# Performance work log

Measured on AMD Instinct MI355X. Metric: run time of the kernel, lower is better.

Reference implementation:

```python
import jax, jax.numpy as jnp
import numpy as np

GAM1 = 1.0
GAM2 = 1.0
EPS = 0.01


def setup_inputs() -> dict:
    key = jax.random.key(0)
    k1, k2 = jax.random.split(key)
    m, p, k = 262144, 128, 10
    x = jax.random.normal(k1, (m, p), dtype=jnp.float32)
    y = jax.random.randint(k2, (m,), 0, k, dtype=jnp.int32)
    return {"x": x, "y": y, "num_classes": k}


def reference(x, y, num_classes):
    m, p = x.shape
    I = jnp.eye(p, dtype=x.dtype)
    scalar = p / (m * EPS)

    # W = x.T, so W @ W.T == x.T @ x  (p x p Gram)
    cov = x.T @ x
    discrimn_empi = jnp.linalg.slogdet(I + GAM1 * scalar * cov)[1] / 2.0
    discrimn_theo = jnp.linalg.slogdet(I + scalar * cov)[1] / 2.0

    # per-class compress loss: logdet(I + p/(n_j*eps) * W_j W_j^T) * n_j / m
    onehot = jax.nn.one_hot(y, num_classes, dtype=x.dtype)  # [m, k]
    counts = onehot.sum(axis=0)                             # [k]

    def class_cov(col):  # col: [m] 0/1 mask for one class
        return (x * col[:, None]).T @ x  # [p, p]

    covs = jax.lax.map(class_cov, onehot.T)  # [k, p, p], sequential over k classes

    safe_counts = jnp.maximum(counts, 1.0)
    scal = p / (safe_counts * EPS)                              # [k]
    lds = jnp.linalg.slogdet(I[None] + scal[:, None, None] * covs)[1]  # [k]
    compress = jnp.sum(jnp.where(counts > 0, lds * counts / m, 0.0)) / 2.0

    total_loss_empi = GAM2 * (-discrimn_empi) + compress
    return total_loss_empi, discrimn_empi, discrimn_theo, compress
```

## Files before the change

kernel.cpp:

```cpp
#include <hip/hip_runtime.h>

#define K 10
#define P 128
#define EPSV 0.01f
#define GAM1 1.0f
#define GAM2 1.0f
#define CH 512
#define SK 64
#define KS 68
#define NSTG (CH / SK)
#define SORTCH 2048
#define NTHR 256
#define GTHR 512

typedef __attribute__((ext_vector_type(8))) short bf16x8;
typedef __attribute__((ext_vector_type(4))) short s16x4;
typedef __attribute__((ext_vector_type(4))) float f32x4;

static __device__ __forceinline__ short f2bf(float f) {
    unsigned u = __float_as_uint(f);
    u = (u + 0x7FFFu + ((u >> 16) & 1u)) >> 16;
    return (short)u;
}

static __device__ __forceinline__ float rdlane(float v, int srclane) {
    return __int_as_float(__builtin_amdgcn_readlane(__float_as_int(v), srclane));
}

__global__ void hist_kernel(const int* __restrict__ y, int* __restrict__ blk_counts, int m) {
    __shared__ int h[K];
    int t = threadIdx.x;
    if (t < K) h[t] = 0;
    __syncthreads();
    int base = blockIdx.x * SORTCH;
    int rows = min(SORTCH, m - base);
    for (int i = t; i < rows; i += NTHR) atomicAdd(&h[y[base + i]], 1);
    __syncthreads();
    if (t < K) blk_counts[blockIdx.x * K + t] = h[t];
}

__global__ void scan_kernel(const int* __restrict__ blk_counts, int* __restrict__ blk_offsets,
                            int* __restrict__ counts, int* __restrict__ pstart, int nb) {
    __shared__ int s[K][128];
    __shared__ int sps[K + 1];
    int t = threadIdx.x;
    int own[K];
    if (t < 128) {
        for (int c = 0; c < K; ++c) {
            int v = (t < nb) ? blk_counts[t * K + c] : 0;
            own[c] = v;
            s[c][t] = v;
        }
    }
    __syncthreads();
    for (int off = 1; off < 128; off <<= 1) {
        int tmp[K];
        if (t < 128)
            for (int c = 0; c < K; ++c) tmp[c] = (t >= off) ? s[c][t - off] : 0;
        __syncthreads();
        if (t < 128)
            for (int c = 0; c < K; ++c) s[c][t] += tmp[c];
        __syncthreads();
    }
    if (t == 0) {
        int run = 0;
        for (int c = 0; c < K; ++c) {
            sps[c] = run;
            int tot = s[c][127];
            counts[c] = tot;
            pstart[c] = run;
            run += ((tot + CH - 1) / CH) * CH;
        }
        sps[K] = run;
        pstart[K] = run;
    }
    __syncthreads();
    if (t < nb)
        for (int c = 0; c < K; ++c)
            blk_offsets[t * K + c] = sps[c] + s[c][t] - own[c];
}

__global__ void scatter_kernel(const int* __restrict__ y, const int* __restrict__ blk_offsets,
                               int* __restrict__ perm, int m) {
    __shared__ int cur[K];
    int t = threadIdx.x;
    if (t < K) cur[t] = blk_offsets[blockIdx.x * K + t];
    __syncthreads();
    int base = blockIdx.x * SORTCH;
    int rows = min(SORTCH, m - base);
    for (int i = t; i < rows; i += NTHR) {
        int row = base + i;
        int pos = atomicAdd(&cur[y[row]], 1);
        perm[pos] = row;
    }
}

__global__ __launch_bounds__(GTHR, 4) void gram_kernel(const float* __restrict__ x,
                                                       const int* __restrict__ perm,
                                                       const int* __restrict__ pstart,
                                                       const int* __restrict__ counts,
                                                       float* __restrict__ partial) {
    __shared__ int pm[CH];
    __shared__ short xsT[2][P * KS];
    int t = threadIdx.x;
    int base = blockIdx.x * CH;
    int cls = 0;
#pragma unroll
    for (int c = 1; c < K; ++c)
        if (base >= pstart[c]) cls = c;
    const int limit = pstart[cls] + counts[cls];
    pm[t] = perm[base + t];

    const int lane = t & 63;
    const int wave = t >> 6;
    const int m16 = lane & 15;
    const int quad = lane >> 4;
    const int wr = wave >> 1;
    const int wc = wave & 1;
    const int c2 = lane;

    f32x4 acc[2][4];
#pragma unroll
    for (int a = 0; a < 2; ++a)
#pragma unroll
        for (int b = 0; b < 4; ++b) acc[a][b] = (f32x4){0.f, 0.f, 0.f, 0.f};

    __syncthreads();

    float2 v[8];
#pragma unroll
    for (int ii = 0; ii < 8; ++ii) {
        int pos = wave * 8 + ii;
        float2 val; val.x = 0.f; val.y = 0.f;
        if (base + pos < limit) {
            int r = pm[pos];
            val = ((const float2*)(x + (size_t)r * P))[c2];
        }
        v[ii] = val;
    }

    for (int s = 0; s < NSTG; ++s) {
        short* xb = &xsT[s & 1][0];
        short b0[8], b1[8];
#pragma unroll
        for (int ii = 0; ii < 8; ++ii) { b0[ii] = f2bf(v[ii].x); b1[ii] = f2bf(v[ii].y); }
        {
            int col0 = 2 * c2, col1 = col0 + 1;
            int kb = wave * 8;
#pragma unroll
            for (int q = 0; q < 2; ++q) {
                s16x4 w0 = {b0[q * 4], b0[q * 4 + 1], b0[q * 4 + 2], b0[q * 4 + 3]};
                s16x4 w1 = {b1[q * 4], b1[q * 4 + 1], b1[q * 4 + 2], b1[q * 4 + 3]};
                *(s16x4*)&xb[col0 * KS + kb + q * 4] = w0;
                *(s16x4*)&xb[col1 * KS + kb + q * 4] = w1;
            }
        }
        __syncthreads();
        if (s + 1 < NSTG) {
            int sb = (s + 1) * SK;
#pragma unroll
            for (int ii = 0; ii < 8; ++ii) {
                int pos = sb + wave * 8 + ii;
                float2 val; val.x = 0.f; val.y = 0.f;
                if (base + pos < limit) {
                    int r = pm[pos];
                    val = ((const float2*)(x + (size_t)r * P))[c2];
                }
                v[ii] = val;
            }
        }
#pragma unroll
        for (int kk = 0; kk < 2; ++kk) {
            int k0 = kk * 32 + quad * 8;
            bf16x8 bfr[4];
#pragma unroll
            for (int b = 0; b < 4; ++b) {
                int colB = wc * 64 + b * 16 + m16;
                union { bf16x8 v8; s16x4 h[2]; } u;
                u.h[0] = *(const s16x4*)&xb[colB * KS + k0];
                u.h[1] = *(const s16x4*)&xb[colB * KS + k0 + 4];
                bfr[b] = u.v8;
            }
#pragma unroll
            for (int a = 0; a < 2; ++a) {
                int colA = wr * 32 + a * 16 + m16;
                union { bf16x8 v8; s16x4 h[2]; } u;
                u.h[0] = *(const s16x4*)&xb[colA * KS + k0];
                u.h[1] = *(const s16x4*)&xb[colA * KS + k0 + 4];
                bf16x8 af = u.v8;
#pragma unroll
                for (int b = 0; b < 4; ++b)
                    acc[a][b] = __builtin_amdgcn_mfma_f32_16x16x32_bf16(af, bfr[b], acc[a][b], 0, 0, 0);
            }
        }
    }
    float* pt = partial + (size_t)blockIdx.x * (P * P);
#pragma unroll
    for (int a = 0; a < 2; ++a)
#pragma unroll
        for (int b = 0; b < 4; ++b)
#pragma unroll
            for (int r = 0; r < 4; ++r) {
                int gi = wr * 32 + a * 16 + quad * 4 + r;
                int gj = wc * 64 + b * 16 + m16;
                pt[gi * P + gj] = acc[a][b][r];
            }
}

__global__ void reduce_kernel(const float* __restrict__ partial, const int* __restrict__ pstart,
                              float* __restrict__ grams) {
    int c = blockIdx.x >> 6;
    int e = ((blockIdx.x & 63) << 8) + threadIdx.x;
    int b0 = pstart[c] / CH;
    int b1 = pstart[c + 1] / CH;
    float s = 0.f;
    for (int b = b0; b < b1; ++b) s += partial[(size_t)b * (P * P) + e];
    grams[(size_t)c * (P * P) + e] = s;
}

__global__ void sum_kernel(const float* __restrict__ grams, float* __restrict__ gsum) {
    int idx = blockIdx.x * 256 + threadIdx.x;
    float s = 0.f;
#pragma unroll
    for (int c = 0; c < K; ++c) s += grams[c * P * P + idx];
    gsum[idx] = s;
}

__global__ __launch_bounds__(256, 1) void logdet_kernel(const float* __restrict__ grams,
                                                        const float* __restrict__ gsum,
                                                        const int* __restrict__ counts,
                                                        float* __restrict__ logd, int m) {
    __shared__ float A[P * P];
    int t = threadIdx.x, b = blockIdx.x;
    float scale;
    if (b == 0) scale = GAM1 * (float)P / ((float)m * EPSV);
    else if (b == 1) scale = (float)P / ((float)m * EPSV);
    else {
        float cnt = (float)counts[b - 2];
        if (cnt < 1.f) cnt = 1.f;
        scale = (float)P / (cnt * EPSV);
    }
    const float* src = (b < 2) ? gsum : (grams + (size_t)(b - 2) * P * P);
    for (int idx = t; idx < P * P; idx += 256) {
        int i = idx >> 7, c = idx & (P - 1);
        int s2 = (i <= c) ? idx : (c * P + i);
        A[idx] = scale * src[s2] + ((i == c) ? 1.f : 0.f);
    }
    __syncthreads();

    const int lane = t & 63;
    const int wid = t >> 6;
    float lsum = 0.f;

    for (int bs = 0; bs < 4; ++bs) {
        const int j0 = bs * 32;
        if (wid == 0) {
            float a[32];
            if (lane < 32) {
#pragma unroll
                for (int cc = 0; cc < 8; ++cc)
                    *(f32x4*)&a[cc * 4] = *(f32x4*)&A[(j0 + lane) * P + j0 + cc * 4];
            } else {
#pragma unroll
                for (int cc = 0; cc < 32; ++cc) a[cc] = 0.f;
            }
            float myinv = 0.f;
#pragma unroll
            for (int tt = 0; tt < 32; ++tt) {
                float utt = rdlane(a[tt], tt);
                float inv = __builtin_amdgcn_rcpf(utt);
                lsum += __logf(utt);
                if (lane == tt) myinv = inv;
                bool act = (lane < 32) && (lane > tt);
                float lm = act ? a[tt] * inv : 0.f;
                if (act) a[tt] = lm;
#pragma unroll
                for (int k2 = tt + 1; k2 < 32; ++k2) {
                    float utk = rdlane(a[k2], tt);
                    a[k2] -= lm * utk;
                }
            }
            if (lane < 32) A[(j0 + lane) * P + j0 + lane] = myinv;

            if (bs < 3) {
                int nc = P - j0 - 32;
                int c0 = j0 + 32 + lane;
                int c1 = c0 + 64;
                bool v0 = lane < nc;
                bool v1 = lane + 64 < nc;
                int c0a = v0 ? c0 : (j0 + 32);
                int c1a = v1 ? c1 : (j0 + 32);
                float ua[32], ub[32];
#pragma unroll
                for (int j = 0; j < 32; ++j) {
                    ua[j] = A[(j0 + j) * P + c0a];
                    ub[j] = A[(j0 + j) * P + c1a];
                }
#pragma unroll
                for (int j = 0; j < 32; ++j) {
#pragma unroll
                    for (int t2 = 0; t2 < j; ++t2) {
                        float ljt = rdlane(a[t2], j);
                        ua[j] -= ljt * ua[t2];
                        ub[j] -= ljt * ub[t2];
                    }
                }
#pragma unroll
                for (int j = 0; j < 32; ++j) {
                    if (v0) A[(j0 + j) * P + c0] = ua[j];
                    if (v1) A[(j0 + j) * P + c1] = ub[j];
                }
            }
        }
        __syncthreads();

        if (bs < 3) {
            int nc = P - j0 - 32;
            int nt = nc >> 2;
            int ntiles = nt * nt;
            for (int tile = t; tile < ntiles; tile += 256) {
                int ti = tile / nt, tk = tile - ti * nt;
                int i0 = j0 + 32 + ti * 4, k0 = j0 + 32 + tk * 4;
                f32x4 acc0 = {0, 0, 0, 0}, acc1 = {0, 0, 0, 0};
                f32x4 acc2 = {0, 0, 0, 0}, acc3 = {0, 0, 0, 0};
#pragma unroll
                for (int j = 0; j < 32; ++j) {
                    const float* row = &A[(j0 + j) * P];
                    float invd = row[j0 + j];
                    f32x4 ui = *(const f32x4*)&row[i0];
                    f32x4 uk = *(const f32x4*)&row[k0];
                    uk *= invd;
                    acc0 += ui[0] * uk;
                    acc1 += ui[1] * uk;
                    acc2 += ui[2] * uk;
                    acc3 += ui[3] * uk;
                }
                f32x4* r0 = (f32x4*)&A[(i0 + 0) * P + k0];
                f32x4* r1 = (f32x4*)&A[(i0 + 1) * P + k0];
                f32x4* r2 = (f32x4*)&A[(i0 + 2) * P + k0];
                f32x4* r3 = (f32x4*)&A[(i0 + 3) * P + k0];
                *r0 -= acc0; *r1 -= acc1; *r2 -= acc2; *r3 -= acc3;
            }
            __syncthreads();
        }
    }
    if (t == 0) logd[b] = lsum;
}

__global__ void final_kernel(const float* __restrict__ logd, const int* __restrict__ counts,
                             float* __restrict__ out, int m) {
    if (threadIdx.x == 0 && blockIdx.x == 0) {
        float empi = 0.5f * logd[0];
        float theo = 0.5f * logd[1];
        float comp = 0.f;
        for (int c = 0; c < K; ++c) {
            float cnt = (float)counts[c];
            if (cnt > 0.f) comp += logd[2 + c] * cnt / (float)m;
        }
        comp *= 0.5f;
        out[0] = GAM2 * (-empi) + comp;
        out[1] = empi;
        out[2] = theo;
        out[3] = comp;
    }
}

extern "C" void kernel_launch(void* const* d_in, const int* in_sizes, int n_in,
                              void* d_out, int out_size, void* d_ws, size_t ws_size,
                              hipStream_t stream) {
    const float* x = (const float*)d_in[0];
    const int* y = (const int*)d_in[1];
    int m = in_sizes[1];
    int nbs = (m + SORTCH - 1) / SORTCH;
    int nbg = (m + CH - 1) / CH + K;

    char* ws = (char*)d_ws;
    float* grams = (float*)ws;
    float* gsum = (float*)(ws + 655360);
    float* logd = (float*)(ws + 720896);
    int* counts = (int*)(ws + 720960);
    int* pstart = (int*)(ws + 721024);
    int* blk_counts = (int*)(ws + 721152);
    int* blk_offsets = (int*)(ws + 721152 + (size_t)nbs * K * 4);
    int* perm = (int*)(ws + 721152 + 2 * (size_t)nbs * K * 4);
    float* partial = (float*)(ws + (2u << 20));


    hist_kernel<<<nbs, NTHR, 0, stream>>>(y, blk_counts, m);
    scan_kernel<<<1, NTHR, 0, stream>>>(blk_counts, blk_offsets, counts, pstart, nbs);
    scatter_kernel<<<nbs, NTHR, 0, stream>>>(y, blk_offsets, perm, m);
    gram_kernel<<<nbg, GTHR, 0, stream>>>(x, perm, pstart, counts, partial);
    reduce_kernel<<<K * (P * P / 256), 256, 0, stream>>>(partial, pstart, grams);
    sum_kernel<<<P * P / 256, 256, 0, stream>>>(grams, gsum);
    logdet_kernel<<<K + 2, 256, 0, stream>>>(grams, gsum, counts, logd, m);
    final_kernel<<<1, 1, 0, stream>>>(logd, counts, (float*)d_out, m);
}
```

Measured before the change: 303.2 us.

## Pre-sort x into bf16 class-contiguous buffer before Gram, fuse sum into reduce

The scatter now records each row's destination position, and a new copy kernel reads x coalesced, converts it to bf16 and writes it into a class-sorted buffer. The Gram kernel then streams contiguous bf16 rows instead of gathering fp32 rows through a permutation. The separate sum kernel is folded into the reduce kernel as an extra class slice. This adds an extra pass that writes about 64MB and reads it back. In exchange the Gram loads are half as wide and no longer indirect, and one launch is removed.

Result: slower. 379.8 us (+25.3%).

```diff
diff --git a/kernel.cpp b/kernel.cpp
--- a/kernel.cpp
+++ b/kernel.cpp
@@ -81,7 +81,7 @@
 }
 
 __global__ void scatter_kernel(const int* __restrict__ y, const int* __restrict__ blk_offsets,
-                               int* __restrict__ perm, int m) {
+                               int* __restrict__ posArr, int m) {
     __shared__ int cur[K];
     int t = threadIdx.x;
     if (t < K) cur[t] = blk_offsets[blockIdx.x * K + t];
@@ -91,16 +91,40 @@
     for (int i = t; i < rows; i += NTHR) {
         int row = base + i;
         int pos = atomicAdd(&cur[y[row]], 1);
-        perm[pos] = row;
-    }
-}
-
-__global__ __launch_bounds__(GTHR, 4) void gram_kernel(const float* __restrict__ x,
-                                                       const int* __restrict__ perm,
+        posArr[row] = pos;
+    }
+}
+
+__global__ __launch_bounds__(NTHR) void copy_kernel(const float* __restrict__ x,
+                                                    const int* __restrict__ posArr,
+                                                    short* __restrict__ xs) {
+    int t = threadIdx.x;
+    int lane = t & 63, wave = t >> 6;
+    int rbase = blockIdx.x * 128;
+#pragma unroll
+    for (int rr = 0; rr < 8; ++rr) {
+        float2 d[4];
+        int p[4];
+#pragma unroll
+        for (int j = 0; j < 4; ++j) {
+            int r = rbase + wave + 4 * (rr * 4 + j);
+            p[j] = posArr[r];
+            d[j] = ((const float2*)(x + (size_t)r * P))[lane];
+        }
+#pragma unroll
+        for (int j = 0; j < 4; ++j) {
+            ushort2 o;
+            o.x = (unsigned short)f2bf(d[j].x);
+            o.y = (unsigned short)f2bf(d[j].y);
+            ((ushort2*)(xs + (size_t)p[j] * P))[lane] = o;
+        }
+    }
+}
+
+__global__ __launch_bounds__(GTHR, 4) void gram_kernel(const short* __restrict__ xs,
                                                        const int* __restrict__ pstart,
                                                        const int* __restrict__ counts,
                                                        float* __restrict__ partial) {
-    __shared__ int pm[CH];
     __shared__ short xsT[2][P * KS];
     int t = threadIdx.x;
     int base = blockIdx.x * CH;
@@ -109,7 +133,6 @@
     for (int c = 1; c < K; ++c)
         if (base >= pstart[c]) cls = c;
     const int limit = pstart[cls] + counts[cls];
-    pm[t] = perm[base + t];
 
     const int lane = t & 63;
     const int wave = t >> 6;
@@ -125,17 +148,12 @@
 #pragma unroll
         for (int b = 0; b < 4; ++b) acc[a][b] = (f32x4){0.f, 0.f, 0.f, 0.f};
 
-    __syncthreads();
-
-    float2 v[8];
+    ushort2 v[8];
 #pragma unroll
     for (int ii = 0; ii < 8; ++ii) {
-        int pos = wave * 8 + ii;
-        float2 val; val.x = 0.f; val.y = 0.f;
-        if (base + pos < limit) {
-            int r = pm[pos];
-            val = ((const float2*)(x + (size_t)r * P))[c2];
-        }
+        int gpos = base + wave * 8 + ii;
+        ushort2 val; val.x = 0; val.y = 0;
+        if (gpos < limit) val = ((const ushort2*)(xs + (size_t)gpos * P))[c2];
         v[ii] = val;
     }
 
@@ -143,7 +161,7 @@
         short* xb = &xsT[s & 1][0];
         short b0[8], b1[8];
 #pragma unroll
-        for (int ii = 0; ii < 8; ++ii) { b0[ii] = f2bf(v[ii].x); b1[ii] = f2bf(v[ii].y); }
+        for (int ii = 0; ii < 8; ++ii) { b0[ii] = (short)v[ii].x; b1[ii] = (short)v[ii].y; }
         {
             int col0 = 2 * c2, col1 = col0 + 1;
             int kb = wave * 8;
@@ -160,12 +178,9 @@
             int sb = (s + 1) * SK;
 #pragma unroll
             for (int ii = 0; ii < 8; ++ii) {
-                int pos = sb + wave * 8 + ii;
-                float2 val; val.x = 0.f; val.y = 0.f;
-                if (base + pos < limit) {
-                    int r = pm[pos];
-                    val = ((const float2*)(x + (size_t)r * P))[c2];
-                }
+                int gpos = base + sb + wave * 8 + ii;
+                ushort2 val; val.x = 0; val.y = 0;
+                if (gpos < limit) val = ((const ushort2*)(xs + (size_t)gpos * P))[c2];
                 v[ii] = val;
             }
         }
@@ -193,7 +208,9 @@
                     acc[a][b] = __builtin_amdgcn_mfma_f32_16x16x32_bf16(af, bfr[b], acc[a][b], 0, 0, 0);
             }
         }
-    }
+        __syncthreads();
+    }
+
     float* pt = partial + (size_t)blockIdx.x * (P * P);
 #pragma unroll
     for (int a = 0; a < 2; ++a)
@@ -208,22 +225,15 @@
 }
 
 __global__ void reduce_kernel(const float* __restrict__ partial, const int* __restrict__ pstart,
-                              float* __restrict__ grams) {
+                              float* __restrict__ grams, float* __restrict__ gsum) {
     int c = blockIdx.x >> 6;
     int e = ((blockIdx.x & 63) << 8) + threadIdx.x;
-    int b0 = pstart[c] / CH;
-    int b1 = pstart[c + 1] / CH;
+    int b0 = (c < K) ? pstart[c] / CH : 0;
+    int b1 = (c < K) ? pstart[c + 1] / CH : pstart[K] / CH;
     float s = 0.f;
     for (int b = b0; b < b1; ++b) s += partial[(size_t)b * (P * P) + e];
-    grams[(size_t)c * (P * P) + e] = s;
-}
-
-__global__ void sum_kernel(const float* __restrict__ grams, float* __restrict__ gsum) {
-    int idx = blockIdx.x * 256 + threadIdx.x;
-    float s = 0.f;
-#pragma unroll
-    for (int c = 0; c < K; ++c) s += grams[c * P * P + idx];
-    gsum[idx] = s;
+    if (c < K) grams[(size_t)c * (P * P) + e] = s;
+    else gsum[e] = s;
 }
 
 __global__ __launch_bounds__(256, 1) void logdet_kernel(const float* __restrict__ grams,
@@ -373,6 +383,7 @@
     int m = in_sizes[1];
     int nbs = (m + SORTCH - 1) / SORTCH;
     int nbg = (m + CH - 1) / CH + K;
+    int nbc = m / 128;
 
     char* ws = (char*)d_ws;
     float* grams = (float*)ws;
@@ -382,16 +393,17 @@
     int* pstart = (int*)(ws + 721024);
     int* blk_counts = (int*)(ws + 721152);
     int* blk_offsets = (int*)(ws + 721152 + (size_t)nbs * K * 4);
-    int* perm = (int*)(ws + 721152 + 2 * (size_t)nbs * K * 4);
-    float* partial = (float*)(ws + (2u << 20));
+    int* posArr = (int*)(ws + (1u << 20));
+    short* xs = (short*)(ws + (2u << 20));
+    float* partial = (float*)(ws + (72u << 20));
 
 
     hist_kernel<<<nbs, NTHR, 0, stream>>>(y, blk_counts, m);
     scan_kernel<<<1, NTHR, 0, stream>>>(blk_counts, blk_offsets, counts, pstart, nbs);
-    scatter_kernel<<<nbs, NTHR, 0, stream>>>(y, blk_offsets, perm, m);
-    gram_kernel<<<nbg, GTHR, 0, stream>>>(x, perm, pstart, counts, partial);
-    reduce_kernel<<<K * (P * P / 256), 256, 0, stream>>>(partial, pstart, grams);
-    sum_kernel<<<P * P / 256, 256, 0, stream>>>(grams, gsum);
+    scatter_kernel<<<nbs, NTHR, 0, stream>>>(y, blk_offsets, posArr, m);
+    copy_kernel<<<nbc, NTHR, 0, stream>>>(x, posArr, xs);
+    gram_kernel<<<nbg, GTHR, 0, stream>>>(xs, pstart, counts, partial);
+    reduce_kernel<<<(K + 1) * (P * P / 256), 256, 0, stream>>>(partial, pstart, grams, gsum);
     logdet_kernel<<<K + 2, 256, 0, stream>>>(grams, gsum, counts, logd, m);
     final_kernel<<<1, 1, 0, stream>>>(logd, counts, (float*)d_out, m);
 }
```

## Halve gram chunk size, widen x loads to float4, fuse gsum into reduce

Applied to the files above, without the earlier changes.

Halves the rows per gram block, so twice as many blocks run and the padding waste per class is smaller. Each lane now loads a float4 of an x row instead of a float2, and the bf16 transpose into LDS is rearranged to match. The separate sum_kernel is removed: extra reduce blocks sum every partial directly into gsum, saving one launch. The cost is a partial buffer twice as large, more reduction traffic, and the gsum blocks re-reading all partials.

Result: slower. 509.7 us (+68.1%).

```diff
diff --git a/kernel.cpp b/kernel.cpp
--- a/kernel.cpp
+++ b/kernel.cpp
@@ -5,7 +5,7 @@
 #define EPSV 0.01f
 #define GAM1 1.0f
 #define GAM2 1.0f
-#define CH 512
+#define CH 256
 #define SK 64
 #define KS 68
 #define NSTG (CH / SK)
@@ -109,7 +109,7 @@
     for (int c = 1; c < K; ++c)
         if (base >= pstart[c]) cls = c;
     const int limit = pstart[cls] + counts[cls];
-    pm[t] = perm[base + t];
+    if (t < CH) pm[t] = perm[base + t];
 
     const int lane = t & 63;
     const int wave = t >> 6;
@@ -117,7 +117,8 @@
     const int quad = lane >> 4;
     const int wr = wave >> 1;
     const int wc = wave & 1;
-    const int c2 = lane;
+    const int hi = lane >> 5;
+    const int l32 = lane & 31;
 
     f32x4 acc[2][4];
 #pragma unroll
@@ -127,44 +128,38 @@
 
     __syncthreads();
 
-    float2 v[8];
-#pragma unroll
-    for (int ii = 0; ii < 8; ++ii) {
-        int pos = wave * 8 + ii;
-        float2 val; val.x = 0.f; val.y = 0.f;
+    f32x4 v[4];
+#pragma unroll
+    for (int ii = 0; ii < 4; ++ii) {
+        int pos = wave * 8 + hi * 4 + ii;
+        f32x4 val = (f32x4){0.f, 0.f, 0.f, 0.f};
         if (base + pos < limit) {
             int r = pm[pos];
-            val = ((const float2*)(x + (size_t)r * P))[c2];
+            val = ((const f32x4*)(x + (size_t)r * P))[l32];
         }
         v[ii] = val;
     }
 
     for (int s = 0; s < NSTG; ++s) {
         short* xb = &xsT[s & 1][0];
-        short b0[8], b1[8];
-#pragma unroll
-        for (int ii = 0; ii < 8; ++ii) { b0[ii] = f2bf(v[ii].x); b1[ii] = f2bf(v[ii].y); }
         {
-            int col0 = 2 * c2, col1 = col0 + 1;
-            int kb = wave * 8;
-#pragma unroll
-            for (int q = 0; q < 2; ++q) {
-                s16x4 w0 = {b0[q * 4], b0[q * 4 + 1], b0[q * 4 + 2], b0[q * 4 + 3]};
-                s16x4 w1 = {b1[q * 4], b1[q * 4 + 1], b1[q * 4 + 2], b1[q * 4 + 3]};
-                *(s16x4*)&xb[col0 * KS + kb + q * 4] = w0;
-                *(s16x4*)&xb[col1 * KS + kb + q * 4] = w1;
+            int kb = wave * 8 + hi * 4;
+#pragma unroll
+            for (int q = 0; q < 4; ++q) {
+                s16x4 w = {f2bf(v[0][q]), f2bf(v[1][q]), f2bf(v[2][q]), f2bf(v[3][q])};
+                *(s16x4*)&xb[(4 * l32 + q) * KS + kb] = w;
             }
         }
         __syncthreads();
         if (s + 1 < NSTG) {
             int sb = (s + 1) * SK;
 #pragma unroll
-            for (int ii = 0; ii < 8; ++ii) {
-                int pos = sb + wave * 8 + ii;
-                float2 val; val.x = 0.f; val.y = 0.f;
+            for (int ii = 0; ii < 4; ++ii) {
+                int pos = sb + wave * 8 + hi * 4 + ii;
+                f32x4 val = (f32x4){0.f, 0.f, 0.f, 0.f};
                 if (base + pos < limit) {
                     int r = pm[pos];
-                    val = ((const float2*)(x + (size_t)r * P))[c2];
+                    val = ((const f32x4*)(x + (size_t)r * P))[l32];
                 }
                 v[ii] = val;
             }
@@ -194,6 +189,7 @@
             }
         }
     }
+
     float* pt = partial + (size_t)blockIdx.x * (P * P);
 #pragma unroll
     for (int a = 0; a < 2; ++a)
@@ -208,22 +204,15 @@
 }
 
 __global__ void reduce_kernel(const float* __restrict__ partial, const int* __restrict__ pstart,
-                              float* __restrict__ grams) {
+                              float* __restrict__ grams, float* __restrict__ gsum) {
     int c = blockIdx.x >> 6;
     int e = ((blockIdx.x & 63) << 8) + threadIdx.x;
-    int b0 = pstart[c] / CH;
-    int b1 = pstart[c + 1] / CH;
+    int b0 = (c < K) ? pstart[c] / CH : 0;
+    int b1 = (c < K) ? pstart[c + 1] / CH : pstart[K] / CH;
     float s = 0.f;
     for (int b = b0; b < b1; ++b) s += partial[(size_t)b * (P * P) + e];
-    grams[(size_t)c * (P * P) + e] = s;
-}
-
-__global__ void sum_kernel(const float* __restrict__ grams, float* __restrict__ gsum) {
-    int idx = blockIdx.x * 256 + threadIdx.x;
-    float s = 0.f;
-#pragma unroll
-    for (int c = 0; c < K; ++c) s += grams[c * P * P + idx];
-    gsum[idx] = s;
+    if (c < K) grams[(size_t)c * (P * P) + e] = s;
+    else gsum[e] = s;
 }
 
 __global__ __launch_bounds__(256, 1) void logdet_kernel(const float* __restrict__ grams,
@@ -390,8 +379,7 @@
     scan_kernel<<<1, NTHR, 0, stream>>>(blk_counts, blk_offsets, counts, pstart, nbs);
     scatter_kernel<<<nbs, NTHR, 0, stream>>>(y, blk_offsets, perm, m);
     gram_kernel<<<nbg, GTHR, 0, stream>>>(x, perm, pstart, counts, partial);
-    reduce_kernel<<<K * (P * P / 256), 256, 0, stream>>>(partial, pstart, grams);
-    sum_kernel<<<P * P / 256, 256, 0, stream>>>(grams, gsum);
+    reduce_kernel<<<(K + 1) * (P * P / 256), 256, 0, stream>>>(partial, pstart, grams, gsum);
     logdet_kernel<<<K + 2, 256, 0, stream>>>(grams, gsum, counts, logd, m);
     final_kernel<<<1, 1, 0, stream>>>(logd, counts, (float*)d_out, m);
 }
```

## Fuse sort stages with grid spin barrier and reduce grams via atomics

Applied to the files above, without the earlier changes.

Merges histogram, scan and scatter into one kernel: the last-arriving block does the scan while the other blocks spin on a flag. The gram kernel now atomically adds its upper-triangle tiles straight into per-class grams, which removes the partial buffer and the reduce kernel. The logdet kernel builds the total Gram itself, and its last-finishing block writes the final outputs. This cuts launches and partial-buffer traffic, but adds a memset, atomic contention, and a spin wait that assumes all sort blocks are co-resident.

Result: slower. 377.8 us (+24.6%).

```diff
diff --git a/kernel.cpp b/kernel.cpp
--- a/kernel.cpp
+++ b/kernel.cpp
@@ -27,8 +27,18 @@
     return __int_as_float(__builtin_amdgcn_readlane(__float_as_int(v), srclane));
 }
 
-__global__ void hist_kernel(const int* __restrict__ y, int* __restrict__ blk_counts, int m) {
+__global__ __launch_bounds__(NTHR) void sort_kernel(const int* __restrict__ y,
+                                                    int* __restrict__ blk_counts,
+                                                    int* __restrict__ blk_offsets,
+                                                    int* __restrict__ counts,
+                                                    int* __restrict__ pstart,
+                                                    int* __restrict__ tick,
+                                                    int* __restrict__ perm, int m, int nb) {
     __shared__ int h[K];
+    __shared__ int s[K][128];
+    __shared__ int sps[K + 1];
+    __shared__ int cur[K];
+    __shared__ int isw;
     int t = threadIdx.x;
     if (t < K) h[t] = 0;
     __syncthreads();
@@ -37,57 +47,60 @@
     for (int i = t; i < rows; i += NTHR) atomicAdd(&h[y[base + i]], 1);
     __syncthreads();
     if (t < K) blk_counts[blockIdx.x * K + t] = h[t];
-}
-
-__global__ void scan_kernel(const int* __restrict__ blk_counts, int* __restrict__ blk_offsets,
-                            int* __restrict__ counts, int* __restrict__ pstart, int nb) {
-    __shared__ int s[K][128];
-    __shared__ int sps[K + 1];
-    int t = threadIdx.x;
-    int own[K];
-    if (t < 128) {
-        for (int c = 0; c < K; ++c) {
-            int v = (t < nb) ? blk_counts[t * K + c] : 0;
-            own[c] = v;
-            s[c][t] = v;
-        }
-    }
-    __syncthreads();
-    for (int off = 1; off < 128; off <<= 1) {
-        int tmp[K];
-        if (t < 128)
-            for (int c = 0; c < K; ++c) tmp[c] = (t >= off) ? s[c][t - off] : 0;
-        __syncthreads();
-        if (t < 128)
-            for (int c = 0; c < K; ++c) s[c][t] += tmp[c];
-        __syncthreads();
-    }
+    __threadfence();
+    __syncthreads();
     if (t == 0) {
-        int run = 0;
-        for (int c = 0; c < K; ++c) {
-            sps[c] = run;
-            int tot = s[c][127];
-            counts[c] = tot;
-            pstart[c] = run;
-            run += ((tot + CH - 1) / CH) * CH;
-        }
-        sps[K] = run;
-        pstart[K] = run;
-    }
-    __syncthreads();
-    if (t < nb)
-        for (int c = 0; c < K; ++c)
-            blk_offsets[t * K + c] = sps[c] + s[c][t] - own[c];
-}
-
-__global__ void scatter_kernel(const int* __restrict__ y, const int* __restrict__ blk_offsets,
-                               int* __restrict__ perm, int m) {
-    __shared__ int cur[K];
-    int t = threadIdx.x;
+        int old = atomicAdd(&tick[0], 1);
+        isw = (old == nb - 1) ? 1 : 0;
+    }
+    __syncthreads();
+    if (isw) {
+        __threadfence();
+        int own[K];
+        if (t < 128) {
+            for (int c = 0; c < K; ++c) {
+                int v = (t < nb) ? blk_counts[t * K + c] : 0;
+                own[c] = v;
+                s[c][t] = v;
+            }
+        }
+        __syncthreads();
+        for (int off = 1; off < 128; off <<= 1) {
+            int tmp[K];
+            if (t < 128)
+                for (int c = 0; c < K; ++c) tmp[c] = (t >= off) ? s[c][t - off] : 0;
+            __syncthreads();
+            if (t < 128)
+                for (int c = 0; c < K; ++c) s[c][t] += tmp[c];
+            __syncthreads();
+        }
+        if (t == 0) {
+            int run = 0;
+            for (int c = 0; c < K; ++c) {
+                sps[c] = run;
+                int tot = s[c][127];
+                counts[c] = tot;
+                pstart[c] = run;
+                run += ((tot + CH - 1) / CH) * CH;
+            }
+            sps[K] = run;
+            pstart[K] = run;
+        }
+        __syncthreads();
+        if (t < nb)
+            for (int c = 0; c < K; ++c)
+                blk_offsets[t * K + c] = sps[c] + s[c][t] - own[c];
+        __threadfence();
+        __syncthreads();
+        if (t == 0) atomicExch(&tick[1], 1);
+    }
+    if (t == 0) {
+        while (atomicAdd(&tick[1], 0) == 0) { __builtin_amdgcn_s_sleep(8); }
+    }
+    __syncthreads();
+    __threadfence();
     if (t < K) cur[t] = blk_offsets[blockIdx.x * K + t];
     __syncthreads();
-    int base = blockIdx.x * SORTCH;
-    int rows = min(SORTCH, m - base);
     for (int i = t; i < rows; i += NTHR) {
         int row = base + i;
         int pos = atomicAdd(&cur[y[row]], 1);
@@ -99,7 +112,7 @@
                                                        const int* __restrict__ perm,
                                                        const int* __restrict__ pstart,
                                                        const int* __restrict__ counts,
-                                                       float* __restrict__ partial) {
+                                                       float* __restrict__ grams) {
     __shared__ int pm[CH];
     __shared__ short xsT[2][P * KS];
     int t = threadIdx.x;
@@ -194,7 +207,8 @@
             }
         }
     }
-    float* pt = partial + (size_t)blockIdx.x * (P * P);
+
+    float* g = grams + (size_t)cls * P * P;
 #pragma unroll
     for (int a = 0; a < 2; ++a)
 #pragma unroll
@@ -203,33 +217,15 @@
             for (int r = 0; r < 4; ++r) {
                 int gi = wr * 32 + a * 16 + quad * 4 + r;
                 int gj = wc * 64 + b * 16 + m16;
-                pt[gi * P + gj] = acc[a][b][r];
-            }
-}
-
-__global__ void reduce_kernel(const float* __restrict__ partial, const int* __restrict__ pstart,
-                              float* __restrict__ grams) {
-    int c = blockIdx.x >> 6;
-    int e = ((blockIdx.x & 63) << 8) + threadIdx.x;
-    int b0 = pstart[c] / CH;
-    int b1 = pstart[c + 1] / CH;
-    float s = 0.f;
-    for (int b = b0; b < b1; ++b) s += partial[(size_t)b * (P * P) + e];
-    grams[(size_t)c * (P * P) + e] = s;
-}
-
-__global__ void sum_kernel(const float* __restrict__ grams, float* __restrict__ gsum) {
-    int idx = blockIdx.x * 256 + threadIdx.x;
-    float s = 0.f;
-#pragma unroll
-    for (int c = 0; c < K; ++c) s += grams[c * P * P + idx];
-    gsum[idx] = s;
+                if (gi <= gj) atomicAdd(&g[gi * P + gj], acc[a][b][r]);
+            }
 }
 
 __global__ __launch_bounds__(256, 1) void logdet_kernel(const float* __restrict__ grams,
-                                                        const float* __restrict__ gsum,
                                                         const int* __restrict__ counts,
-                                                        float* __restrict__ logd, int m) {
+                                                        float* __restrict__ logd,
+                                                        int* __restrict__ tick,
+                                                        float* __restrict__ out, int m) {
     __shared__ float A[P * P];
     int t = threadIdx.x, b = blockIdx.x;
     float scale;
@@ -240,11 +236,18 @@
         if (cnt < 1.f) cnt = 1.f;
         scale = (float)P / (cnt * EPSV);
     }
-    const float* src = (b < 2) ? gsum : (grams + (size_t)(b - 2) * P * P);
     for (int idx = t; idx < P * P; idx += 256) {
         int i = idx >> 7, c = idx & (P - 1);
         int s2 = (i <= c) ? idx : (c * P + i);
-        A[idx] = scale * src[s2] + ((i == c) ? 1.f : 0.f);
+        float sv;
+        if (b < 2) {
+            sv = 0.f;
+#pragma unroll
+            for (int cc = 0; cc < K; ++cc) sv += grams[cc * P * P + s2];
+        } else {
+            sv = grams[(size_t)(b - 2) * P * P + s2];
+        }
+        A[idx] = scale * sv + ((i == c) ? 1.f : 0.f);
     }
     __syncthreads();
 
@@ -344,24 +347,27 @@
             __syncthreads();
         }
     }
-    if (t == 0) logd[b] = lsum;
-}
-
-__global__ void final_kernel(const float* __restrict__ logd, const int* __restrict__ counts,
-                             float* __restrict__ out, int m) {
-    if (threadIdx.x == 0 && blockIdx.x == 0) {
-        float empi = 0.5f * logd[0];
-        float theo = 0.5f * logd[1];
-        float comp = 0.f;
-        for (int c = 0; c < K; ++c) {
-            float cnt = (float)counts[c];
-            if (cnt > 0.f) comp += logd[2 + c] * cnt / (float)m;
-        }
-        comp *= 0.5f;
-        out[0] = GAM2 * (-empi) + comp;
-        out[1] = empi;
-        out[2] = theo;
-        out[3] = comp;
+    if (t == 0) {
+        logd[b] = lsum;
+        __threadfence();
+        int old = atomicAdd(&tick[2], 1);
+        if (old == (int)gridDim.x - 1) {
+            float ld[K + 2];
+#pragma unroll
+            for (int i = 0; i < K + 2; ++i) ld[i] = atomicAdd(&logd[i], 0.0f);
+            float empi = 0.5f * ld[0];
+            float theo = 0.5f * ld[1];
+            float comp = 0.f;
+            for (int c = 0; c < K; ++c) {
+                float cnt = (float)counts[c];
+                if (cnt > 0.f) comp += ld[2 + c] * cnt / (float)m;
+            }
+            comp *= 0.5f;
+            out[0] = GAM2 * (-empi) + comp;
+            out[1] = empi;
+            out[2] = theo;
+            out[3] = comp;
+        }
     }
 }
 
@@ -376,22 +382,18 @@
 
     char* ws = (char*)d_ws;
     float* grams = (float*)ws;
-    float* gsum = (float*)(ws + 655360);
-    float* logd = (float*)(ws + 720896);
-    int* counts = (int*)(ws + 720960);
-    int* pstart = (int*)(ws + 721024);
-    int* blk_counts = (int*)(ws + 721152);
-    int* blk_offsets = (int*)(ws + 721152 + (size_t)nbs * K * 4);
-    int* perm = (int*)(ws + 721152 + 2 * (size_t)nbs * K * 4);
-    float* partial = (float*)(ws + (2u << 20));
-
-
-    hist_kernel<<<nbs, NTHR, 0, stream>>>(y, blk_counts, m);
-    scan_kernel<<<1, NTHR, 0, stream>>>(blk_counts, blk_offsets, counts, pstart, nbs);
-    scatter_kernel<<<nbs, NTHR, 0, stream>>>(y, blk_offsets, perm, m);
-    gram_kernel<<<nbg, GTHR, 0, stream>>>(x, perm, pstart, counts, partial);
-    reduce_kernel<<<K * (P * P / 256), 256, 0, stream>>>(partial, pstart, grams);
-    sum_kernel<<<P * P / 256, 256, 0, stream>>>(grams, gsum);
-    logdet_kernel<<<K + 2, 256, 0, stream>>>(grams, gsum, counts, logd, m);
-    final_kernel<<<1, 1, 0, stream>>>(logd, counts, (float*)d_out, m);
-}
+    int* tick = (int*)(ws + 655360);
+    int* counts = (int*)(ws + 655424);
+    int* pstart = (int*)(ws + 655488);
+    float* logd = (float*)(ws + 655552);
+    int* blk_counts = (int*)(ws + 655616);
+    int* blk_offsets = (int*)(ws + 660736);
+    int* perm = (int*)(ws + 665856);
+
+    hipMemsetAsync(ws, 0, 655376, stream);
+
+    sort_kernel<<<nbs, NTHR, 0, stream>>>(y, blk_counts, blk_offsets, counts, pstart,
+                                          tick, perm, m, nbs);
+    gram_kernel<<<nbg, GTHR, 0, stream>>>(x, perm, pstart, counts, grams);
+    logdet_kernel<<<K + 2, 256, 0, stream>>>(grams, counts, logd, tick, (float*)d_out, m);
+}
```
